# Kernel optimization log

Measured on AMD Instinct MI355X. Metric: run time of the kernel, lower is better.

## Reference

```python
import jax, jax.numpy as jnp
import numpy as np

HEADS = 8
DIM_HEAD = 32
EPS = 1e-5


def _rel_index(h, w):
    # matches Attention._generate_relative_index (static, computed on host)
    coords = np.stack(np.meshgrid(np.arange(h), np.arange(w), indexing='ij')).reshape(2, -1)
    rel = coords[:, :, None] - coords[:, None, :]  # [2, n, n]
    rel[0] += h - 1
    rel[1] += w - 1
    rel[0] *= 2 * w - 1
    idx = rel.sum(0).reshape(-1)
    # torch.clamp(relative_index, 0, max_index) -- indices are already in range here
    return jnp.asarray(np.clip(idx, 0, (2 * h - 1) * (2 * w - 1) - 1))


def _layernorm(x, g, b):
    m = jnp.mean(x, axis=-1, keepdims=True)
    v = jnp.var(x, axis=-1, keepdims=True)
    return (x - m) * jax.lax.rsqrt(v + EPS) * g + b


def setup_inputs() -> dict:
    key = jax.random.key(0)
    ks = jax.random.split(key, 6)
    B, C, H, W = 64, 384, 16, 16
    inner = HEADS * DIM_HEAD  # 256
    hid = 4 * C               # 1536
    def nrm(k, shape, s=0.02):
        return jax.random.normal(k, shape, jnp.float32) * s
    return {
        'x': jax.random.normal(ks[0], (B, C, H, W), jnp.float32),
        'ln1_g': jnp.ones((C,), jnp.float32),
        'ln1_b': jnp.zeros((C,), jnp.float32),
        'w_qkv': nrm(ks[1], (C, 3 * inner)),
        'bias_table': nrm(ks[2], ((2 * H - 1) * (2 * W - 1), HEADS)),
        'w_out': nrm(ks[3], (inner, C)),
        'b_out': jnp.zeros((C,), jnp.float32),
        'ln2_g': jnp.ones((C,), jnp.float32),
        'ln2_b': jnp.zeros((C,), jnp.float32),
        'w_ff1': nrm(ks[4], (C, hid)),
        'b_ff1': jnp.zeros((hid,), jnp.float32),
        'w_ff2': nrm(ks[5], (hid, C)),
        'b_ff2': jnp.zeros((C,), jnp.float32),
    }


def reference(x, ln1_g, ln1_b, w_qkv, bias_table, w_out, b_out,
              ln2_g, ln2_b, w_ff1, b_ff1, w_ff2, b_ff2):
    B, C, H, W = x.shape
    n = H * W
    t = x.reshape(B, C, n).transpose(0, 2, 1)  # [B, n, C]

    # --- attention branch (PreNorm(LayerNorm) -> Attention) ---
    a = _layernorm(t, ln1_g, ln1_b)
    qkv = a @ w_qkv  # [B, n, 3*inner]
    q, k, v = jnp.split(qkv, 3, axis=-1)
    def split_heads(z):
        return z.reshape(B, n, HEADS, DIM_HEAD).transpose(0, 2, 1, 3)  # [B, h, n, d]
    q, k, v = split_heads(q), split_heads(k), split_heads(v)
    dots = jnp.einsum('bhid,bhjd->bhij', q, k) * (DIM_HEAD ** -0.5)
    idx = _rel_index(H, W)  # [n*n]
    rel_bias = bias_table[idx].reshape(n, n, HEADS).transpose(2, 0, 1)[None]  # [1, h, n, n]
    attn = jax.nn.softmax(dots + rel_bias, axis=-1)
    o = jnp.einsum('bhij,bhjd->bhid', attn, v)
    o = o.transpose(0, 2, 1, 3).reshape(B, n, HEADS * DIM_HEAD)
    attn_out = o @ w_out + b_out  # to_out Linear (dropout=0)

    # --- feedforward branch (PreNorm(LayerNorm) -> FFN) ---
    f = _layernorm(t, ln2_g, ln2_b)
    f = jax.nn.gelu(f @ w_ff1 + b_ff1, approximate=False) @ w_ff2 + b_ff2

    y = t + attn_out + f  # x_adjusted + attn_out + ff_out
    return y.transpose(0, 2, 1).reshape(B, C, H, W)
```

## Files before the change

### kernel.cpp

```cpp
#include <hip/hip_runtime.h>

typedef __bf16 bf16;
typedef __bf16 bf16x8 __attribute__((ext_vector_type(8)));
typedef float f32x4 __attribute__((ext_vector_type(4)));

__device__ __forceinline__ void gll16(const void* g, void* l) {
    __builtin_amdgcn_global_load_lds((const __attribute__((address_space(1))) void*)g,
                                     (__attribute__((address_space(3))) void*)l, 16, 0, 0);
}

__device__ __forceinline__ float gelu_f(float v) {
    float u = v * (0.7978845608028654f + 0.03567740814183074f * v * v);
    float t = __expf(-2.0f * fabsf(u));
    float th = (1.0f - t) / (1.0f + t);
    th = copysignf(th, u);
    return 0.5f * v * (1.0f + th);
}

__launch_bounds__(256)
__global__ void transpose_all(const float* __restrict__ wqkv, const float* __restrict__ wout,
                              const float* __restrict__ wff1, const float* __restrict__ wff2,
                              bf16* __restrict__ wqkvT, bf16* __restrict__ woutT,
                              bf16* __restrict__ wff1T, bf16* __restrict__ wff2T) {
    __shared__ float tl[32][33];
    int g = blockIdx.x;
    const float* in; bf16* out; int R, Cc, bx, by;
    if (g < 288)       { in = wqkv; out = wqkvT; R = 384;  Cc = 768;  bx = g % 24; by = g / 24; }
    else if (g < 384)  { g -= 288; in = wout; out = woutT; R = 256;  Cc = 384;  bx = g % 12; by = g / 12; }
    else if (g < 960)  { g -= 384; in = wff1; out = wff1T; R = 384;  Cc = 1536; bx = g % 48; by = g / 48; }
    else               { g -= 960; in = wff2; out = wff2T; R = 1536; Cc = 384;  bx = g % 12; by = g / 12; }
    const int c0 = bx * 32, r0 = by * 32;
    const int cl = threadIdx.x & 31, r8 = threadIdx.x >> 5;
#pragma unroll
    for (int k = 0; k < 4; k++) {
        int r = k * 8 + r8;
        tl[r][cl] = in[(size_t)(r0 + r) * Cc + c0 + cl];
    }
    __syncthreads();
#pragma unroll
    for (int k = 0; k < 4; k++) {
        int cc = k * 8 + r8;
        out[(size_t)(c0 + cc) * R + r0 + cl] = (bf16)tl[cl][cc];
    }
}

__launch_bounds__(256)
__global__ void ln_kernel(const float* __restrict__ x,
                          const float* __restrict__ g1, const float* __restrict__ b1,
                          const float* __restrict__ g2, const float* __restrict__ b2,
                          bf16* __restrict__ a, bf16* __restrict__ f) {
    __shared__ float tile[384][33];
    __shared__ float S[8][32], SS[8][32], Mn[32], Rs[32];
    const int tid = threadIdx.x;
    const int bb = blockIdx.x >> 3;
    const int chunk = blockIdx.x & 7;
    const int i0 = chunk * 32;
    {
        const int i_l = tid & 31, c_l = tid >> 5;
        const size_t base = (size_t)bb * 384 * 256 + i0 + i_l;
#pragma unroll 6
        for (int c = c_l; c < 384; c += 8)
            tile[c][i_l] = x[base + (size_t)c * 256];
    }
    __syncthreads();
    {
        const int i_s = tid & 31, p = tid >> 5;
        float s = 0.f, ss = 0.f;
#pragma unroll 6
        for (int j = 0; j < 48; j++) {
            float v = tile[p * 48 + j][i_s];
            s += v; ss += v * v;
        }
        S[p][i_s] = s; SS[p][i_s] = ss;
    }
    __syncthreads();
    if (tid < 32) {
        float t1 = 0.f, t2 = 0.f;
#pragma unroll
        for (int p = 0; p < 8; p++) { t1 += S[p][tid]; t2 += SS[p][tid]; }
        float mean = t1 * (1.0f / 384.0f);
        float var  = t2 * (1.0f / 384.0f) - mean * mean;
        Mn[tid] = mean;
        Rs[tid] = rsqrtf(var + 1e-5f);
    }
    __syncthreads();
    const int lane = tid & 63, w = tid >> 6;
#pragma unroll
    for (int rr = 0; rr < 8; rr++) {
        const int i = w * 8 + rr;
        const float mean = Mn[i], rstd = Rs[i];
        const size_t orow = ((size_t)bb * 256 + i0 + i) * 384;
#pragma unroll
        for (int pass = 0; pass < 6; pass++) {
            const int c = pass * 64 + lane;
            float nh = (tile[c][i] - mean) * rstd;
            a[orow + c] = (bf16)(nh * g1[c] + b1[c]);
            f[orow + c] = (bf16)(nh * g2[c] + b2[c]);
        }
    }
}

#define GEMM_PROLOGUE_AND_KLOOP                                                     \
    const int tid = threadIdx.x;                                                    \
    const int g = blockIdx.x;                                                       \
    const int x_ = (g >> 3) % nx;                                                   \
    const int y_ = (g & 7) + 8 * (g / (8 * nx));                                    \
    const int m0 = y_ * 128, n0 = x_ * 128;                                         \
    const int lane = tid & 63, w = tid >> 6;                                        \
    const int l16 = lane & 15, quad = lane >> 4;                                    \
    const int wm = (w & 1) * 64, wn = (w >> 1) * 64;                                \
    f32x4 zero = {0.f, 0.f, 0.f, 0.f};                                              \
    f32x4 acc[4][4];                                                                \
    _Pragma("unroll") for (int i = 0; i < 4; i++)                                   \
        _Pragma("unroll") for (int j = 0; j < 4; j++) acc[i][j] = zero;             \
    const int c0 = tid, c1 = tid + 256;                                             \
    const int r0 = c0 >> 2, k0c = (c0 & 3) * 8;                                     \
    const int r1 = c1 >> 2, k1c = (c1 & 3) * 8;                                     \
    const bf16* Abase = A + (size_t)m0 * K;                                         \
    const bf16* Bbase = Bt + (size_t)n0 * K;                                        \
    for (int kb = 0; kb < K; kb += 32) {                                            \
        gll16(Abase + (size_t)r0 * K + kb + k0c, lA + c0 * 8);                      \
        gll16(Abase + (size_t)r1 * K + kb + k1c, lA + c1 * 8);                      \
        gll16(Bbase + (size_t)r0 * K + kb + k0c, lB + c0 * 8);                      \
        gll16(Bbase + (size_t)r1 * K + kb + k1c, lB + c1 * 8);                      \
        __syncthreads();                                                            \
        bf16x8 af[4], bfr[4];                                                       \
        _Pragma("unroll") for (int i = 0; i < 4; i++)                               \
            af[i] = *(const bf16x8*)(lA + (wm + i * 16 + l16) * 32 + quad * 8);     \
        _Pragma("unroll") for (int j = 0; j < 4; j++)                               \
            bfr[j] = *(const bf16x8*)(lB + (wn + j * 16 + l16) * 32 + quad * 8);    \
        _Pragma("unroll") for (int i = 0; i < 4; i++)                               \
            _Pragma("unroll") for (int j = 0; j < 4; j++)                           \
                acc[i][j] = __builtin_amdgcn_mfma_f32_16x16x32_bf16(af[i], bfr[j], acc[i][j], 0, 0, 0); \
        __syncthreads();                                                            \
    }

template <int EPI>
__launch_bounds__(256)
__global__ void gemm_bt(const bf16* __restrict__ A, const bf16* __restrict__ Bt,
                        const float* __restrict__ bias, bf16* __restrict__ C,
                        int M, int N, int K, int nx) {
    __shared__ bf16 lds[16384];
    bf16* lA = lds;
    bf16* lB = lds + 4096;
    GEMM_PROLOGUE_AND_KLOOP
#pragma unroll
    for (int j = 0; j < 4; j++) {
        const int col = wn + j * 16 + l16;
        float bv = 0.f;
        if (EPI >= 1) bv = bias[n0 + col];
#pragma unroll
        for (int i = 0; i < 4; i++) {
            const int row0 = wm + i * 16 + quad * 4;
#pragma unroll
            for (int r = 0; r < 4; r++) {
                float v = acc[i][j][r] + bv;
                if (EPI == 2) v = gelu_f(v);
                lds[(row0 + r) * 128 + col] = (bf16)v;
            }
        }
    }
    __syncthreads();
#pragma unroll
    for (int it = 0; it < 8; it++) {
        const int ch = tid + it * 256;
        const int row = ch >> 4, cc = (ch & 15) * 8;
        *(bf16x8*)(C + (size_t)(m0 + row) * N + n0 + cc) = *(const bf16x8*)(lds + row * 128 + cc);
    }
}

__launch_bounds__(256)
__global__ void gemm_bt_tr(const bf16* __restrict__ A, const bf16* __restrict__ Bt,
                           const float* __restrict__ bias, bf16* __restrict__ Ct,
                           int M, int N, int K, int nx) {
    __shared__ bf16 lds[128 * 132];
    bf16* lA = lds;
    bf16* lB = lds + 4096;
    GEMM_PROLOGUE_AND_KLOOP
#pragma unroll
    for (int j = 0; j < 4; j++) {
        const int col = wn + j * 16 + l16;
        const float bv = bias[n0 + col];
#pragma unroll
        for (int i = 0; i < 4; i++) {
            const int row0 = wm + i * 16 + quad * 4;
#pragma unroll
            for (int r = 0; r < 4; r++)
                lds[col * 132 + row0 + r] = (bf16)(acc[i][j][r] + bv);
        }
    }
    __syncthreads();
    const int b = m0 >> 8, ib = m0 & 255;
#pragma unroll
    for (int it = 0; it < 8; it++) {
        const int ch = tid + it * 256;
        const int cl = ch >> 4, ic = (ch & 15) * 8;
        *(bf16x8*)(Ct + ((size_t)(b * 384 + n0 + cl) * 256 + ib + ic)) =
            *(const bf16x8*)(lds + cl * 132 + ic);
    }
}

__launch_bounds__(256)
__global__ void gemm_bt_final(const bf16* __restrict__ A, const bf16* __restrict__ Bt,
                              const float* __restrict__ bias,
                              const float* __restrict__ xres, const bf16* __restrict__ attn_t,
                              float* __restrict__ out, int M, int N, int K, int nx) {
    __shared__ bf16 lds[128 * 132];
    bf16* lA = lds;
    bf16* lB = lds + 4096;
    GEMM_PROLOGUE_AND_KLOOP
#pragma unroll
    for (int j = 0; j < 4; j++) {
        const int col = wn + j * 16 + l16;
        const float bv = bias[n0 + col];
#pragma unroll
        for (int i = 0; i < 4; i++) {
            const int row0 = wm + i * 16 + quad * 4;
#pragma unroll
            for (int r = 0; r < 4; r++)
                lds[col * 132 + row0 + r] = (bf16)(acc[i][j][r] + bv);
        }
    }
    __syncthreads();
    const int b = m0 >> 8, ib = m0 & 255;
#pragma unroll
    for (int it = 0; it < 8; it++) {
        const int ch = tid + it * 256;
        const int cl = ch >> 4, ic = (ch & 15) * 8;
        const size_t base = (size_t)(b * 384 + n0 + cl) * 256 + ib + ic;
        bf16x8 ff = *(const bf16x8*)(lds + cl * 132 + ic);
        bf16x8 at = *(const bf16x8*)(attn_t + base);
#pragma unroll
        for (int e = 0; e < 8; e++)
            out[base + e] = xres[base + e] + (float)at[e] + (float)ff[e];
    }
}

__launch_bounds__(256)
__global__ void attn_kernel(const bf16* __restrict__ qkv,
                            const float* __restrict__ btab,
                            bf16* __restrict__ o) {
    __shared__ float sbias[961];
    __shared__ __align__(16) bf16 sVt[32][264];
    __shared__ __align__(16) bf16 sP[4][16][264];
    const int tid = threadIdx.x;
    const int qc = blockIdx.x & 3;
    const int h  = (blockIdx.x >> 2) & 7;
    const int bb = blockIdx.x >> 5;
    const int lane = tid & 63, w = tid >> 6;
    const int l16 = lane & 15, quad = lane >> 4;
    const size_t qkvb = (size_t)bb * 256 * 768;

    for (int e = tid; e < 961; e += 256) sbias[e] = btab[e * 8 + h];
#pragma unroll
    for (int it = 0; it < 32; it++) {
        int e = it * 256 + tid;
        int k = e >> 5, d = e & 31;
        sVt[d][k] = qkv[qkvb + (size_t)k * 768 + 512 + h * 32 + d];
    }
    __syncthreads();

    const int qbase = qc * 64 + w * 16;
    bf16x8 qf = *(const bf16x8*)(qkv + qkvb + (size_t)(qbase + l16) * 768 + h * 32 + quad * 8);
    f32x4 zero = {0.f, 0.f, 0.f, 0.f};
    f32x4 s[16];
#pragma unroll
    for (int kt = 0; kt < 16; kt++) {
        bf16x8 kf = *(const bf16x8*)(qkv + qkvb + (size_t)(kt * 16 + l16) * 768 + 256 + h * 32 + quad * 8);
        s[kt] = __builtin_amdgcn_mfma_f32_16x16x32_bf16(qf, kf, zero, 0, 0, 0);
    }
    const int qi0 = qbase + quad * 4;
    float mx[4] = {-1e30f, -1e30f, -1e30f, -1e30f};
#pragma unroll
    for (int kt = 0; kt < 16; kt++) {
        const int j = kt * 16 + l16;
        const int yj = j >> 4, xj = j & 15;
#pragma unroll
        for (int r = 0; r < 4; r++) {
            const int q = qi0 + r;
            const int tix = ((q >> 4) - yj + 15) * 31 + ((q & 15) - xj + 15);
            float v = s[kt][r] * 0.17677669529663687f + sbias[tix];
            s[kt][r] = v;
            mx[r] = fmaxf(mx[r], v);
        }
    }
#pragma unroll
    for (int r = 0; r < 4; r++)
        for (int msk = 1; msk < 16; msk <<= 1)
            mx[r] = fmaxf(mx[r], __shfl_xor(mx[r], msk, 64));
    float sum[4] = {0.f, 0.f, 0.f, 0.f};
#pragma unroll
    for (int kt = 0; kt < 16; kt++)
#pragma unroll
        for (int r = 0; r < 4; r++) {
            float e = __expf(s[kt][r] - mx[r]);
            s[kt][r] = e;
            sum[r] += e;
        }
#pragma unroll
    for (int r = 0; r < 4; r++) {
        for (int msk = 1; msk < 16; msk <<= 1)
            sum[r] += __shfl_xor(sum[r], msk, 64);
        sum[r] = 1.0f / sum[r];
    }
#pragma unroll
    for (int kt = 0; kt < 16; kt++)
#pragma unroll
        for (int r = 0; r < 4; r++)
            sP[w][quad * 4 + r][kt * 16 + l16] = (bf16)(s[kt][r] * sum[r]);
    f32x4 oacc[2];
    oacc[0] = zero; oacc[1] = zero;
#pragma unroll
    for (int ks = 0; ks < 8; ks++) {
        bf16x8 pf = *(const bf16x8*)(&sP[w][l16][ks * 32 + quad * 8]);
#pragma unroll
        for (int dt = 0; dt < 2; dt++) {
            bf16x8 vf = *(const bf16x8*)(&sVt[dt * 16 + l16][ks * 32 + quad * 8]);
            oacc[dt] = __builtin_amdgcn_mfma_f32_16x16x32_bf16(pf, vf, oacc[dt], 0, 0, 0);
        }
    }
#pragma unroll
    for (int dt = 0; dt < 2; dt++)
#pragma unroll
        for (int r = 0; r < 4; r++)
            o[(size_t)(bb * 256 + qbase + quad * 4 + r) * 256 + h * 32 + dt * 16 + l16] = (bf16)oacc[dt][r];
}

extern "C" void kernel_launch(void* const* d_in, const int* in_sizes, int n_in,
                              void* d_out, int out_size, void* d_ws, size_t ws_size,
                              hipStream_t stream) {
    const float* x    = (const float*)d_in[0];
    const float* g1   = (const float*)d_in[1];
    const float* b1   = (const float*)d_in[2];
    const float* wqkv = (const float*)d_in[3];
    const float* btab = (const float*)d_in[4];
    const float* wout = (const float*)d_in[5];
    const float* bout = (const float*)d_in[6];
    const float* g2   = (const float*)d_in[7];
    const float* b2   = (const float*)d_in[8];
    const float* wff1 = (const float*)d_in[9];
    const float* bff1 = (const float*)d_in[10];
    const float* wff2 = (const float*)d_in[11];
    const float* bff2 = (const float*)d_in[12];
    float* out = (float*)d_out;

    bf16* ws = (bf16*)d_ws;
    const size_t NA = 6291456;
    bf16* wqkvT = ws;
    bf16* woutT = wqkvT + 294912;
    bf16* wff1T = woutT + 98304;
    bf16* wff2T = wff1T + 589824;
    bf16* f_buf    = ws + 1572864;
    bf16* attn_t   = f_buf + NA;
    bf16* R        = attn_t + NA;
    bf16* a_buf    = R;
    bf16* qkv_buf  = R + NA;
    bf16* o_buf    = R;
    bf16* ffh_buf  = R;

    dim3 b256(256);
    transpose_all<<<1536, b256, 0, stream>>>(wqkv, wout, wff1, wff2, wqkvT, woutT, wff1T, wff2T);

    ln_kernel<<<512, b256, 0, stream>>>(x, g1, b1, g2, b2, a_buf, f_buf);

    gemm_bt<0><<<6 * 128, b256, 0, stream>>>(a_buf, wqkvT, nullptr, qkv_buf, 16384, 768, 384, 6);
    attn_kernel<<<2048, b256, 0, stream>>>(qkv_buf, btab, o_buf);
    gemm_bt_tr<<<3 * 128, b256, 0, stream>>>(o_buf, woutT, bout, attn_t, 16384, 384, 256, 3);
    gemm_bt<2><<<12 * 128, b256, 0, stream>>>(f_buf, wff1T, bff1, ffh_buf, 16384, 1536, 384, 12);
    gemm_bt_final<<<3 * 128, b256, 0, stream>>>(ffh_buf, wff2T, bff2, x, attn_t, out,
                                                16384, 384, 1536, 3);
}
```

Before: 274.7 us.

## Merge weight transpose with layernorm and halve GEMM epilogue LDS footprint

Fuses the weight-transpose and layernorm kernels into one launch to save a kernel launch and let both run concurrently. GEMM epilogues now stage the output tile in two halves, shrinking shared memory per block (32KB to 16KB, ~33KB to ~17KB) to raise occupancy. In gemm_bt the GELU is moved to the vectorized store pass. Trade-off is an extra barrier per epilogue and warps idling during half the staging; the fused prep kernel also uses the larger LDS size for transpose blocks.

```diff
diff --git a/kernel.cpp b/kernel.cpp
--- a/kernel.cpp
+++ b/kernel.cpp
@@ -18,43 +18,47 @@
 }
 
 __launch_bounds__(256)
-__global__ void transpose_all(const float* __restrict__ wqkv, const float* __restrict__ wout,
-                              const float* __restrict__ wff1, const float* __restrict__ wff2,
-                              bf16* __restrict__ wqkvT, bf16* __restrict__ woutT,
-                              bf16* __restrict__ wff1T, bf16* __restrict__ wff2T) {
-    __shared__ float tl[32][33];
+__global__ void prep_kernel(const float* __restrict__ wqkv, const float* __restrict__ wout,
+                            const float* __restrict__ wff1, const float* __restrict__ wff2,
+                            bf16* __restrict__ wqkvT, bf16* __restrict__ woutT,
+                            bf16* __restrict__ wff1T, bf16* __restrict__ wff2T,
+                            const float* __restrict__ x,
+                            const float* __restrict__ g1, const float* __restrict__ b1,
+                            const float* __restrict__ g2, const float* __restrict__ b2,
+                            bf16* __restrict__ a, bf16* __restrict__ f) {
+    __shared__ __align__(16) float smem[12672 + 512 + 64];
+    const int tid = threadIdx.x;
     int g = blockIdx.x;
-    const float* in; bf16* out; int R, Cc, bx, by;
-    if (g < 288)       { in = wqkv; out = wqkvT; R = 384;  Cc = 768;  bx = g % 24; by = g / 24; }
-    else if (g < 384)  { g -= 288; in = wout; out = woutT; R = 256;  Cc = 384;  bx = g % 12; by = g / 12; }
-    else if (g < 960)  { g -= 384; in = wff1; out = wff1T; R = 384;  Cc = 1536; bx = g % 48; by = g / 48; }
-    else               { g -= 960; in = wff2; out = wff2T; R = 1536; Cc = 384;  bx = g % 12; by = g / 12; }
-    const int c0 = bx * 32, r0 = by * 32;
-    const int cl = threadIdx.x & 31, r8 = threadIdx.x >> 5;
-#pragma unroll
-    for (int k = 0; k < 4; k++) {
-        int r = k * 8 + r8;
-        tl[r][cl] = in[(size_t)(r0 + r) * Cc + c0 + cl];
-    }
-    __syncthreads();
-#pragma unroll
-    for (int k = 0; k < 4; k++) {
-        int cc = k * 8 + r8;
-        out[(size_t)(c0 + cc) * R + r0 + cl] = (bf16)tl[cl][cc];
-    }
-}
-
-__launch_bounds__(256)
-__global__ void ln_kernel(const float* __restrict__ x,
-                          const float* __restrict__ g1, const float* __restrict__ b1,
-                          const float* __restrict__ g2, const float* __restrict__ b2,
-                          bf16* __restrict__ a, bf16* __restrict__ f) {
-    __shared__ float tile[384][33];
-    __shared__ float S[8][32], SS[8][32], Mn[32], Rs[32];
-    const int tid = threadIdx.x;
-    const int bb = blockIdx.x >> 3;
-    const int chunk = blockIdx.x & 7;
-    const int i0 = chunk * 32;
+    if (g < 1536) {
+        float (*tl)[33] = (float (*)[33])smem;
+        const float* in; bf16* out; int R, Cc, bx, by;
+        if (g < 288)       { in = wqkv; out = wqkvT; R = 384;  Cc = 768;  bx = g % 24; by = g / 24; }
+        else if (g < 384)  { g -= 288; in = wout; out = woutT; R = 256;  Cc = 384;  bx = g % 12; by = g / 12; }
+        else if (g < 960)  { g -= 384; in = wff1; out = wff1T; R = 384;  Cc = 1536; bx = g % 48; by = g / 48; }
+        else               { g -= 960; in = wff2; out = wff2T; R = 1536; Cc = 384;  bx = g % 12; by = g / 12; }
+        const int c0 = bx * 32, r0 = by * 32;
+        const int cl = tid & 31, r8 = tid >> 5;
+#pragma unroll
+        for (int k = 0; k < 4; k++) {
+            int r = k * 8 + r8;
+            tl[r][cl] = in[(size_t)(r0 + r) * Cc + c0 + cl];
+        }
+        __syncthreads();
+#pragma unroll
+        for (int k = 0; k < 4; k++) {
+            int cc = k * 8 + r8;
+            out[(size_t)(c0 + cc) * R + r0 + cl] = (bf16)tl[cl][cc];
+        }
+        return;
+    }
+    g -= 1536;
+    float (*tile)[33] = (float (*)[33])smem;
+    float (*S)[32]  = (float (*)[32])(smem + 12672);
+    float (*SS)[32] = (float (*)[32])(smem + 12928);
+    float* Mn = smem + 13184;
+    float* Rs = smem + 13216;
+    const int bb = g >> 3;
+    const int i0 = (g & 7) * 32;
     {
         const int i_l = tid & 31, c_l = tid >> 5;
         const size_t base = (size_t)bb * 384 * 256 + i0 + i_l;
@@ -140,32 +144,40 @@
 __global__ void gemm_bt(const bf16* __restrict__ A, const bf16* __restrict__ Bt,
                         const float* __restrict__ bias, bf16* __restrict__ C,
                         int M, int N, int K, int nx) {
-    __shared__ bf16 lds[16384];
+    __shared__ bf16 lds[8192];
     bf16* lA = lds;
     bf16* lB = lds + 4096;
     GEMM_PROLOGUE_AND_KLOOP
 #pragma unroll
-    for (int j = 0; j < 4; j++) {
-        const int col = wn + j * 16 + l16;
-        float bv = 0.f;
-        if (EPI >= 1) bv = bias[n0 + col];
-#pragma unroll
-        for (int i = 0; i < 4; i++) {
-            const int row0 = wm + i * 16 + quad * 4;
-#pragma unroll
-            for (int r = 0; r < 4; r++) {
-                float v = acc[i][j][r] + bv;
-                if (EPI == 2) v = gelu_f(v);
-                lds[(row0 + r) * 128 + col] = (bf16)v;
+    for (int hh = 0; hh < 2; hh++) {
+        if ((w & 1) == hh) {
+#pragma unroll
+            for (int j = 0; j < 4; j++) {
+                const int col = wn + j * 16 + l16;
+                float bv = 0.f;
+                if (EPI >= 1) bv = bias[n0 + col];
+#pragma unroll
+                for (int i = 0; i < 4; i++) {
+                    const int row0 = i * 16 + quad * 4;
+#pragma unroll
+                    for (int r = 0; r < 4; r++)
+                        lds[(row0 + r) * 128 + col] = (bf16)(acc[i][j][r] + bv);
+                }
             }
         }
-    }
-    __syncthreads();
-#pragma unroll
-    for (int it = 0; it < 8; it++) {
-        const int ch = tid + it * 256;
-        const int row = ch >> 4, cc = (ch & 15) * 8;
-        *(bf16x8*)(C + (size_t)(m0 + row) * N + n0 + cc) = *(const bf16x8*)(lds + row * 128 + cc);
+        __syncthreads();
+#pragma unroll
+        for (int it = 0; it < 4; it++) {
+            const int ch = tid + it * 256;
+            const int row = ch >> 4, cc = (ch & 15) * 8;
+            bf16x8 vv = *(const bf16x8*)(lds + row * 128 + cc);
+            if (EPI == 2) {
+#pragma unroll
+                for (int e = 0; e < 8; e++) vv[e] = (bf16)gelu_f((float)vv[e]);
+            }
+            *(bf16x8*)(C + (size_t)(m0 + hh * 64 + row) * N + n0 + cc) = vv;
+        }
+        if (hh == 0) __syncthreads();
     }
 }
 
@@ -173,30 +185,36 @@
 __global__ void gemm_bt_tr(const bf16* __restrict__ A, const bf16* __restrict__ Bt,
                            const float* __restrict__ bias, bf16* __restrict__ Ct,
                            int M, int N, int K, int nx) {
-    __shared__ bf16 lds[128 * 132];
+    __shared__ bf16 lds[8448];
     bf16* lA = lds;
     bf16* lB = lds + 4096;
     GEMM_PROLOGUE_AND_KLOOP
-#pragma unroll
-    for (int j = 0; j < 4; j++) {
-        const int col = wn + j * 16 + l16;
-        const float bv = bias[n0 + col];
-#pragma unroll
-        for (int i = 0; i < 4; i++) {
-            const int row0 = wm + i * 16 + quad * 4;
-#pragma unroll
-            for (int r = 0; r < 4; r++)
-                lds[col * 132 + row0 + r] = (bf16)(acc[i][j][r] + bv);
-        }
-    }
-    __syncthreads();
     const int b = m0 >> 8, ib = m0 & 255;
 #pragma unroll
-    for (int it = 0; it < 8; it++) {
-        const int ch = tid + it * 256;
-        const int cl = ch >> 4, ic = (ch & 15) * 8;
-        *(bf16x8*)(Ct + ((size_t)(b * 384 + n0 + cl) * 256 + ib + ic)) =
-            *(const bf16x8*)(lds + cl * 132 + ic);
+    for (int hh = 0; hh < 2; hh++) {
+        if ((w >> 1) == hh) {
+#pragma unroll
+            for (int j = 0; j < 4; j++) {
+                const int lcol = j * 16 + l16;
+                const float bv = bias[n0 + hh * 64 + lcol];
+#pragma unroll
+                for (int i = 0; i < 4; i++) {
+                    const int row0 = wm + i * 16 + quad * 4;
+#pragma unroll
+                    for (int r = 0; r < 4; r++)
+                        lds[lcol * 132 + row0 + r] = (bf16)(acc[i][j][r] + bv);
+                }
+            }
+        }
+        __syncthreads();
+#pragma unroll
+        for (int it = 0; it < 4; it++) {
+            const int ch = tid + it * 256;
+            const int cl = ch >> 4, ic = (ch & 15) * 8;
+            *(bf16x8*)(Ct + ((size_t)(b * 384 + n0 + hh * 64 + cl) * 256 + ib + ic)) =
+                *(const bf16x8*)(lds + cl * 132 + ic);
+        }
+        if (hh == 0) __syncthreads();
     }
 }
 
@@ -205,34 +223,40 @@
                               const float* __restrict__ bias,
                               const float* __restrict__ xres, const bf16* __restrict__ attn_t,
                               float* __restrict__ out, int M, int N, int K, int nx) {
-    __shared__ bf16 lds[128 * 132];
+    __shared__ bf16 lds[8448];
     bf16* lA = lds;
     bf16* lB = lds + 4096;
     GEMM_PROLOGUE_AND_KLOOP
-#pragma unroll
-    for (int j = 0; j < 4; j++) {
-        const int col = wn + j * 16 + l16;
-        const float bv = bias[n0 + col];
-#pragma unroll
-        for (int i = 0; i < 4; i++) {
-            const int row0 = wm + i * 16 + quad * 4;
-#pragma unroll
-            for (int r = 0; r < 4; r++)
-                lds[col * 132 + row0 + r] = (bf16)(acc[i][j][r] + bv);
-        }
-    }
-    __syncthreads();
     const int b = m0 >> 8, ib = m0 & 255;
 #pragma unroll
-    for (int it = 0; it < 8; it++) {
-        const int ch = tid + it * 256;
-        const int cl = ch >> 4, ic = (ch & 15) * 8;
-        const size_t base = (size_t)(b * 384 + n0 + cl) * 256 + ib + ic;
-        bf16x8 ff = *(const bf16x8*)(lds + cl * 132 + ic);
-        bf16x8 at = *(const bf16x8*)(attn_t + base);
-#pragma unroll
-        for (int e = 0; e < 8; e++)
-            out[base + e] = xres[base + e] + (float)at[e] + (float)ff[e];
+    for (int hh = 0; hh < 2; hh++) {
+        if ((w >> 1) == hh) {
+#pragma unroll
+            for (int j = 0; j < 4; j++) {
+                const int lcol = j * 16 + l16;
+                const float bv = bias[n0 + hh * 64 + lcol];
+#pragma unroll
+                for (int i = 0; i < 4; i++) {
+                    const int row0 = wm + i * 16 + quad * 4;
+#pragma unroll
+                    for (int r = 0; r < 4; r++)
+                        lds[lcol * 132 + row0 + r] = (bf16)(acc[i][j][r] + bv);
+                }
+            }
+        }
+        __syncthreads();
+#pragma unroll
+        for (int it = 0; it < 4; it++) {
+            const int ch = tid + it * 256;
+            const int cl = ch >> 4, ic = (ch & 15) * 8;
+            const size_t base = (size_t)(b * 384 + n0 + hh * 64 + cl) * 256 + ib + ic;
+            bf16x8 ff = *(const bf16x8*)(lds + cl * 132 + ic);
+            bf16x8 at = *(const bf16x8*)(attn_t + base);
+#pragma unroll
+            for (int e = 0; e < 8; e++)
+                out[base + e] = xres[base + e] + (float)at[e] + (float)ff[e];
+        }
+        if (hh == 0) __syncthreads();
     }
 }
 
@@ -359,9 +383,8 @@
     bf16* ffh_buf  = R;
 
     dim3 b256(256);
-    transpose_all<<<1536, b256, 0, stream>>>(wqkv, wout, wff1, wff2, wqkvT, woutT, wff1T, wff2T);
-
-    ln_kernel<<<512, b256, 0, stream>>>(x, g1, b1, g2, b2, a_buf, f_buf);
+    prep_kernel<<<2048, b256, 0, stream>>>(wqkv, wout, wff1, wff2, wqkvT, woutT, wff1T, wff2T,
+                                           x, g1, b1, g2, b2, a_buf, f_buf);
 
     gemm_bt<0><<<6 * 128, b256, 0, stream>>>(a_buf, wqkvT, nullptr, qkv_buf, 16384, 768, 384, 6);
     attn_kernel<<<2048, b256, 0, stream>>>(qkv_buf, btab, o_buf);
```

New measurement: 281.4 us. 2.5% more time.

## Merge weight prep with layernorm, narrow N-tiles for N=384 GEMMs, use exact erf GELU

Applied to the files above, without the earlier changes.

Folds the weight transpose and the layernorm into one prep kernel launch. The two GEMMs with N=384 (out projection and FF2) now use 128x64 tiles, doubling their grid from 384 to 768 blocks so more CUs are filled. The GELU epilogue switches from a tanh approximation to erff, which matches the reference more closely but may cost more per element. The narrower tiles load more A per unit of output, reducing data reuse.

```diff
diff --git a/kernel.cpp b/kernel.cpp
--- a/kernel.cpp
+++ b/kernel.cpp
@@ -9,52 +9,48 @@
                                      (__attribute__((address_space(3))) void*)l, 16, 0, 0);
 }
 
-__device__ __forceinline__ float gelu_f(float v) {
-    float u = v * (0.7978845608028654f + 0.03567740814183074f * v * v);
-    float t = __expf(-2.0f * fabsf(u));
-    float th = (1.0f - t) / (1.0f + t);
-    th = copysignf(th, u);
-    return 0.5f * v * (1.0f + th);
-}
-
 __launch_bounds__(256)
-__global__ void transpose_all(const float* __restrict__ wqkv, const float* __restrict__ wout,
-                              const float* __restrict__ wff1, const float* __restrict__ wff2,
-                              bf16* __restrict__ wqkvT, bf16* __restrict__ woutT,
-                              bf16* __restrict__ wff1T, bf16* __restrict__ wff2T) {
-    __shared__ float tl[32][33];
+__global__ void prep_kernel(const float* __restrict__ wqkv, const float* __restrict__ wout,
+                            const float* __restrict__ wff1, const float* __restrict__ wff2,
+                            bf16* __restrict__ wqkvT, bf16* __restrict__ woutT,
+                            bf16* __restrict__ wff1T, bf16* __restrict__ wff2T,
+                            const float* __restrict__ x,
+                            const float* __restrict__ g1, const float* __restrict__ b1,
+                            const float* __restrict__ g2, const float* __restrict__ b2,
+                            bf16* __restrict__ a, bf16* __restrict__ f) {
+    __shared__ __align__(16) float smem[12672 + 512 + 64];
+    const int tid = threadIdx.x;
     int g = blockIdx.x;
-    const float* in; bf16* out; int R, Cc, bx, by;
-    if (g < 288)       { in = wqkv; out = wqkvT; R = 384;  Cc = 768;  bx = g % 24; by = g / 24; }
-    else if (g < 384)  { g -= 288; in = wout; out = woutT; R = 256;  Cc = 384;  bx = g % 12; by = g / 12; }
-    else if (g < 960)  { g -= 384; in = wff1; out = wff1T; R = 384;  Cc = 1536; bx = g % 48; by = g / 48; }
-    else               { g -= 960; in = wff2; out = wff2T; R = 1536; Cc = 384;  bx = g % 12; by = g / 12; }
-    const int c0 = bx * 32, r0 = by * 32;
-    const int cl = threadIdx.x & 31, r8 = threadIdx.x >> 5;
-#pragma unroll
-    for (int k = 0; k < 4; k++) {
-        int r = k * 8 + r8;
-        tl[r][cl] = in[(size_t)(r0 + r) * Cc + c0 + cl];
-    }
-    __syncthreads();
-#pragma unroll
-    for (int k = 0; k < 4; k++) {
-        int cc = k * 8 + r8;
-        out[(size_t)(c0 + cc) * R + r0 + cl] = (bf16)tl[cl][cc];
-    }
-}
-
-__launch_bounds__(256)
-__global__ void ln_kernel(const float* __restrict__ x,
-                          const float* __restrict__ g1, const float* __restrict__ b1,
-                          const float* __restrict__ g2, const float* __restrict__ b2,
-                          bf16* __restrict__ a, bf16* __restrict__ f) {
-    __shared__ float tile[384][33];
-    __shared__ float S[8][32], SS[8][32], Mn[32], Rs[32];
-    const int tid = threadIdx.x;
-    const int bb = blockIdx.x >> 3;
-    const int chunk = blockIdx.x & 7;
-    const int i0 = chunk * 32;
+    if (g < 1536) {
+        float (*tl)[33] = (float (*)[33])smem;
+        const float* in; bf16* out; int R, Cc, bx, by;
+        if (g < 288)       { in = wqkv; out = wqkvT; R = 384;  Cc = 768;  bx = g % 24; by = g / 24; }
+        else if (g < 384)  { g -= 288; in = wout; out = woutT; R = 256;  Cc = 384;  bx = g % 12; by = g / 12; }
+        else if (g < 960)  { g -= 384; in = wff1; out = wff1T; R = 384;  Cc = 1536; bx = g % 48; by = g / 48; }
+        else               { g -= 960; in = wff2; out = wff2T; R = 1536; Cc = 384;  bx = g % 12; by = g / 12; }
+        const int c0 = bx * 32, r0 = by * 32;
+        const int cl = tid & 31, r8 = tid >> 5;
+#pragma unroll
+        for (int k = 0; k < 4; k++) {
+            int r = k * 8 + r8;
+            tl[r][cl] = in[(size_t)(r0 + r) * Cc + c0 + cl];
+        }
+        __syncthreads();
+#pragma unroll
+        for (int k = 0; k < 4; k++) {
+            int cc = k * 8 + r8;
+            out[(size_t)(c0 + cc) * R + r0 + cl] = (bf16)tl[cl][cc];
+        }
+        return;
+    }
+    g -= 1536;
+    float (*tile)[33] = (float (*)[33])smem;
+    float (*S)[32]  = (float (*)[32])(smem + 12672);
+    float (*SS)[32] = (float (*)[32])(smem + 12928);
+    float* Mn = smem + 13184;
+    float* Rs = smem + 13216;
+    const int bb = g >> 3;
+    const int i0 = (g & 7) * 32;
     {
         const int i_l = tid & 31, c_l = tid >> 5;
         const size_t base = (size_t)bb * 384 * 256 + i0 + i_l;
@@ -100,19 +96,95 @@
     }
 }
 
-#define GEMM_PROLOGUE_AND_KLOOP                                                     \
+template <int EPI>
+__launch_bounds__(256)
+__global__ void gemm_bt(const bf16* __restrict__ A, const bf16* __restrict__ Bt,
+                        const float* __restrict__ bias, bf16* __restrict__ C,
+                        int M, int N, int K, int nx) {
+    __shared__ bf16 lds[16384];
+    bf16* lA = lds;
+    bf16* lB = lds + 4096;
+    const int tid = threadIdx.x;
+    const int g = blockIdx.x;
+    const int x = (g >> 3) % nx;
+    const int y = (g & 7) + 8 * (g / (8 * nx));
+    const int m0 = y * 128, n0 = x * 128;
+    const int lane = tid & 63, w = tid >> 6;
+    const int l16 = lane & 15, quad = lane >> 4;
+    const int wm = (w & 1) * 64, wn = (w >> 1) * 64;
+
+    f32x4 zero = {0.f, 0.f, 0.f, 0.f};
+    f32x4 acc[4][4];
+#pragma unroll
+    for (int i = 0; i < 4; i++)
+#pragma unroll
+        for (int j = 0; j < 4; j++) acc[i][j] = zero;
+
+    const int c0 = tid, c1 = tid + 256;
+    const int r0 = c0 >> 2, k0c = (c0 & 3) * 8;
+    const int r1 = c1 >> 2, k1c = (c1 & 3) * 8;
+    const bf16* Abase = A + (size_t)m0 * K;
+    const bf16* Bbase = Bt + (size_t)n0 * K;
+
+    for (int kb = 0; kb < K; kb += 32) {
+        gll16(Abase + (size_t)r0 * K + kb + k0c, lA + c0 * 8);
+        gll16(Abase + (size_t)r1 * K + kb + k1c, lA + c1 * 8);
+        gll16(Bbase + (size_t)r0 * K + kb + k0c, lB + c0 * 8);
+        gll16(Bbase + (size_t)r1 * K + kb + k1c, lB + c1 * 8);
+        __syncthreads();
+        bf16x8 af[4], bfr[4];
+#pragma unroll
+        for (int i = 0; i < 4; i++)
+            af[i] = *(const bf16x8*)(lA + (wm + i * 16 + l16) * 32 + quad * 8);
+#pragma unroll
+        for (int j = 0; j < 4; j++)
+            bfr[j] = *(const bf16x8*)(lB + (wn + j * 16 + l16) * 32 + quad * 8);
+#pragma unroll
+        for (int i = 0; i < 4; i++)
+#pragma unroll
+            for (int j = 0; j < 4; j++)
+                acc[i][j] = __builtin_amdgcn_mfma_f32_16x16x32_bf16(af[i], bfr[j], acc[i][j], 0, 0, 0);
+        __syncthreads();
+    }
+
+#pragma unroll
+    for (int j = 0; j < 4; j++) {
+        const int col = wn + j * 16 + l16;
+        float bv = 0.f;
+        if (EPI >= 1) bv = bias[n0 + col];
+#pragma unroll
+        for (int i = 0; i < 4; i++) {
+            const int row0 = wm + i * 16 + quad * 4;
+#pragma unroll
+            for (int r = 0; r < 4; r++) {
+                float v = acc[i][j][r] + bv;
+                if (EPI == 2) v = 0.5f * v * (1.0f + erff(v * 0.70710678118654752f));
+                lds[(row0 + r) * 128 + col] = (bf16)v;
+            }
+        }
+    }
+    __syncthreads();
+#pragma unroll
+    for (int it = 0; it < 8; it++) {
+        const int ch = tid + it * 256;
+        const int row = ch >> 4, cc = (ch & 15) * 8;
+        *(bf16x8*)(C + (size_t)(m0 + row) * N + n0 + cc) = *(const bf16x8*)(lds + row * 128 + cc);
+    }
+}
+
+#define GEMM64_PROLOGUE_AND_KLOOP                                                   \
     const int tid = threadIdx.x;                                                    \
     const int g = blockIdx.x;                                                       \
     const int x_ = (g >> 3) % nx;                                                   \
     const int y_ = (g & 7) + 8 * (g / (8 * nx));                                    \
-    const int m0 = y_ * 128, n0 = x_ * 128;                                         \
+    const int m0 = y_ * 128, n0 = x_ * 64;                                          \
     const int lane = tid & 63, w = tid >> 6;                                        \
     const int l16 = lane & 15, quad = lane >> 4;                                    \
-    const int wm = (w & 1) * 64, wn = (w >> 1) * 64;                                \
+    const int wm = (w & 1) * 64, wn = (w >> 1) * 32;                                \
     f32x4 zero = {0.f, 0.f, 0.f, 0.f};                                              \
-    f32x4 acc[4][4];                                                                \
+    f32x4 acc[4][2];                                                                \
     _Pragma("unroll") for (int i = 0; i < 4; i++)                                   \
-        _Pragma("unroll") for (int j = 0; j < 4; j++) acc[i][j] = zero;             \
+        _Pragma("unroll") for (int j = 0; j < 2; j++) acc[i][j] = zero;             \
     const int c0 = tid, c1 = tid + 256;                                             \
     const int r0 = c0 >> 2, k0c = (c0 & 3) * 8;                                     \
     const int r1 = c1 >> 2, k1c = (c1 & 3) * 8;                                     \
@@ -122,69 +194,34 @@
         gll16(Abase + (size_t)r0 * K + kb + k0c, lA + c0 * 8);                      \
         gll16(Abase + (size_t)r1 * K + kb + k1c, lA + c1 * 8);                      \
         gll16(Bbase + (size_t)r0 * K + kb + k0c, lB + c0 * 8);                      \
-        gll16(Bbase + (size_t)r1 * K + kb + k1c, lB + c1 * 8);                      \
         __syncthreads();                                                            \
-        bf16x8 af[4], bfr[4];                                                       \
+        bf16x8 af[4], bfr[2];                                                       \
         _Pragma("unroll") for (int i = 0; i < 4; i++)                               \
             af[i] = *(const bf16x8*)(lA + (wm + i * 16 + l16) * 32 + quad * 8);     \
-        _Pragma("unroll") for (int j = 0; j < 4; j++)                               \
+        _Pragma("unroll") for (int j = 0; j < 2; j++)                               \
             bfr[j] = *(const bf16x8*)(lB + (wn + j * 16 + l16) * 32 + quad * 8);    \
         _Pragma("unroll") for (int i = 0; i < 4; i++)                               \
-            _Pragma("unroll") for (int j = 0; j < 4; j++)                           \
+            _Pragma("unroll") for (int j = 0; j < 2; j++)                           \
                 acc[i][j] = __builtin_amdgcn_mfma_f32_16x16x32_bf16(af[i], bfr[j], acc[i][j], 0, 0, 0); \
         __syncthreads();                                                            \
     }
 
-template <int EPI>
 __launch_bounds__(256)
-__global__ void gemm_bt(const bf16* __restrict__ A, const bf16* __restrict__ Bt,
-                        const float* __restrict__ bias, bf16* __restrict__ C,
-                        int M, int N, int K, int nx) {
-    __shared__ bf16 lds[16384];
+__global__ void gemm_bt_tr64(const bf16* __restrict__ A, const bf16* __restrict__ Bt,
+                             const float* __restrict__ bias, bf16* __restrict__ Ct,
+                             int M, int N, int K, int nx) {
+    __shared__ bf16 lds[8448];
     bf16* lA = lds;
     bf16* lB = lds + 4096;
-    GEMM_PROLOGUE_AND_KLOOP
-#pragma unroll
-    for (int j = 0; j < 4; j++) {
+    GEMM64_PROLOGUE_AND_KLOOP
+#pragma unroll
+    for (int j = 0; j < 2; j++) {
         const int col = wn + j * 16 + l16;
-        float bv = 0.f;
-        if (EPI >= 1) bv = bias[n0 + col];
+        const float bv = bias[n0 + col];
 #pragma unroll
         for (int i = 0; i < 4; i++) {
             const int row0 = wm + i * 16 + quad * 4;
 #pragma unroll
-            for (int r = 0; r < 4; r++) {
-                float v = acc[i][j][r] + bv;
-                if (EPI == 2) v = gelu_f(v);
-                lds[(row0 + r) * 128 + col] = (bf16)v;
-            }
-        }
-    }
-    __syncthreads();
-#pragma unroll
-    for (int it = 0; it < 8; it++) {
-        const int ch = tid + it * 256;
-        const int row = ch >> 4, cc = (ch & 15) * 8;
-        *(bf16x8*)(C + (size_t)(m0 + row) * N + n0 + cc) = *(const bf16x8*)(lds + row * 128 + cc);
-    }
-}
-
-__launch_bounds__(256)
-__global__ void gemm_bt_tr(const bf16* __restrict__ A, const bf16* __restrict__ Bt,
-                           const float* __restrict__ bias, bf16* __restrict__ Ct,
-                           int M, int N, int K, int nx) {
-    __shared__ bf16 lds[128 * 132];
-    bf16* lA = lds;
-    bf16* lB = lds + 4096;
-    GEMM_PROLOGUE_AND_KLOOP
-#pragma unroll
-    for (int j = 0; j < 4; j++) {
-        const int col = wn + j * 16 + l16;
-        const float bv = bias[n0 + col];
-#pragma unroll
-        for (int i = 0; i < 4; i++) {
-            const int row0 = wm + i * 16 + quad * 4;
-#pragma unroll
             for (int r = 0; r < 4; r++)
                 lds[col * 132 + row0 + r] = (bf16)(acc[i][j][r] + bv);
         }
@@ -192,7 +229,7 @@
     __syncthreads();
     const int b = m0 >> 8, ib = m0 & 255;
 #pragma unroll
-    for (int it = 0; it < 8; it++) {
+    for (int it = 0; it < 4; it++) {
         const int ch = tid + it * 256;
         const int cl = ch >> 4, ic = (ch & 15) * 8;
         *(bf16x8*)(Ct + ((size_t)(b * 384 + n0 + cl) * 256 + ib + ic)) =
@@ -201,16 +238,16 @@
 }
 
 __launch_bounds__(256)
-__global__ void gemm_bt_final(const bf16* __restrict__ A, const bf16* __restrict__ Bt,
-                              const float* __restrict__ bias,
-                              const float* __restrict__ xres, const bf16* __restrict__ attn_t,
-                              float* __restrict__ out, int M, int N, int K, int nx) {
-    __shared__ bf16 lds[128 * 132];
+__global__ void gemm_bt_final64(const bf16* __restrict__ A, const bf16* __restrict__ Bt,
+                                const float* __restrict__ bias,
+                                const float* __restrict__ xres, const bf16* __restrict__ attn_t,
+                                float* __restrict__ out, int M, int N, int K, int nx) {
+    __shared__ bf16 lds[8448];
     bf16* lA = lds;
     bf16* lB = lds + 4096;
-    GEMM_PROLOGUE_AND_KLOOP
-#pragma unroll
-    for (int j = 0; j < 4; j++) {
+    GEMM64_PROLOGUE_AND_KLOOP
+#pragma unroll
+    for (int j = 0; j < 2; j++) {
         const int col = wn + j * 16 + l16;
         const float bv = bias[n0 + col];
 #pragma unroll
@@ -224,7 +261,7 @@
     __syncthreads();
     const int b = m0 >> 8, ib = m0 & 255;
 #pragma unroll
-    for (int it = 0; it < 8; it++) {
+    for (int it = 0; it < 4; it++) {
         const int ch = tid + it * 256;
         const int cl = ch >> 4, ic = (ch & 15) * 8;
         const size_t base = (size_t)(b * 384 + n0 + cl) * 256 + ib + ic;
@@ -359,14 +396,13 @@
     bf16* ffh_buf  = R;
 
     dim3 b256(256);
-    transpose_all<<<1536, b256, 0, stream>>>(wqkv, wout, wff1, wff2, wqkvT, woutT, wff1T, wff2T);
-
-    ln_kernel<<<512, b256, 0, stream>>>(x, g1, b1, g2, b2, a_buf, f_buf);
+    prep_kernel<<<2048, b256, 0, stream>>>(wqkv, wout, wff1, wff2, wqkvT, woutT, wff1T, wff2T,
+                                           x, g1, b1, g2, b2, a_buf, f_buf);
 
     gemm_bt<0><<<6 * 128, b256, 0, stream>>>(a_buf, wqkvT, nullptr, qkv_buf, 16384, 768, 384, 6);
     attn_kernel<<<2048, b256, 0, stream>>>(qkv_buf, btab, o_buf);
-    gemm_bt_tr<<<3 * 128, b256, 0, stream>>>(o_buf, woutT, bout, attn_t, 16384, 384, 256, 3);
+    gemm_bt_tr64<<<6 * 128, b256, 0, stream>>>(o_buf, woutT, bout, attn_t, 16384, 384, 256, 6);
     gemm_bt<2><<<12 * 128, b256, 0, stream>>>(f_buf, wff1T, bff1, ffh_buf, 16384, 1536, 384, 12);
-    gemm_bt_final<<<3 * 128, b256, 0, stream>>>(ffh_buf, wff2T, bff2, x, attn_t, out,
-                                                16384, 384, 1536, 3);
-}
+    gemm_bt_final64<<<6 * 128, b256, 0, stream>>>(ffh_buf, wff2T, bff2, x, attn_t, out,
+                                                  16384, 384, 1536, 6);
+}
```

Result: faster. 261.8 us (-4.7%).
